# Performance work log

Hardware: AMD Instinct MI355X
Metric: run time of the kernel (lower is better)

Reference implementation:

```python
import jax, jax.numpy as jnp
import numpy as np

GAMMA = 2.0
CONTEXT_WINDOW = 100


def setup_inputs() -> dict:
    key = jax.random.key(0)
    k1, k2 = jax.random.split(key)
    B, S, C = 64, 131072, 3
    inputs = jax.random.normal(k1, (B, S, C), dtype=jnp.float32)
    targets = jax.random.randint(k2, (B, S), 0, C, dtype=jnp.int32)
    alpha = jnp.array([0.25, 1.0, 1.0], dtype=jnp.float32)
    return {"inputs": inputs, "targets": targets, "alpha": alpha}


def _window_mask(targets, window):
    # mask[b, i] = True iff any positive target within +/- window of i;
    # rows with no positives are fully True (matches torch loop semantics).
    B, S = targets.shape
    pos = targets > 0                                   # (B, S) bool
    cs = jnp.cumsum(pos.astype(jnp.int32), axis=1)      # inclusive prefix sums
    c = jnp.concatenate([jnp.zeros((B, 1), jnp.int32), cs], axis=1)  # (B, S+1)
    idx = jnp.arange(S)
    hi = jnp.minimum(idx + window + 1, S)               # exclusive end
    lo = jnp.maximum(idx - window, 0)                   # inclusive start
    count = c[:, hi] - c[:, lo]                         # positives in window
    mask = count > 0
    has_pos = pos.any(axis=1, keepdims=True)
    return jnp.where(has_pos, mask, True)


def reference(inputs, targets, alpha):
    # inputs: (B, S, C) logits; targets: (B, S) class indices
    mask = _window_mask(targets, CONTEXT_WINDOW)                     # (B, S)
    logp = jax.nn.log_softmax(inputs, axis=-1)                       # (B, S, C)
    ce = -jnp.take_along_axis(logp, targets[..., None].astype(jnp.int32), axis=-1)[..., 0]
    p_t = jnp.exp(-ce)
    focal = alpha[targets] * (1.0 - p_t) ** GAMMA * ce               # (B, S)
    m = mask.astype(inputs.dtype)
    # masked mean == mean over selected elements in the torch version
    return jnp.sum(focal * m) / jnp.sum(m)
```

## Files before the change

### kernel.cpp

```cpp
#include <hip/hip_runtime.h>

#define BB 64
#define SS 131072
#define WIN 100
#define TILE 4096
#define NTHREADS 256
#define NWAVES (NTHREADS / 64)
#define TILES_PER_ROW (SS / TILE)
#define NBLOCKS (BB * TILES_PER_ROW)
#define EXT (TILE + 2*WIN)
#define NWORDS ((EXT + 63) / 64)
#define SH_BYTES (NWORDS * 64)
#define K4TOT (SH_BYTES / 4)
#define SROUNDS ((K4TOT + NTHREADS - 1) / NTHREADS)
#define WGROUPS 4
#define GF4 192

typedef float  fx4 __attribute__((ext_vector_type(4)));
typedef int    ix4 __attribute__((ext_vector_type(4)));

__device__ __forceinline__ void process4(
    const fx4 c0, const fx4 c1, const fx4 c2,
    const int j0, const unsigned long long mw, const unsigned int tpack,
    const float a0, const float a1, const float a2,
    float& fsum_m, float& fsum_a, int& cnt_m)
{
    const float xs[12] = {c0.x, c0.y, c0.z, c0.w, c1.x, c1.y, c1.z, c1.w,
                          c2.x, c2.y, c2.z, c2.w};
    #pragma unroll
    for (int j = 0; j < 4; ++j) {
        const float x0 = xs[3*j], x1 = xs[3*j+1], x2 = xs[3*j+2];
        const int tv = (tpack >> (8 * j)) & 0xFF;
        const float mx = fmaxf(x0, fmaxf(x1, x2));
        const float mn = fminf(x0, fminf(x1, x2));
        const float md = fmaxf(fminf(x0, x1), fminf(fmaxf(x0, x1), x2));
        const float emd = __expf(md - mx);
        const float emn = __expf(mn - mx);
        const float sum = 1.0f + emd + emn;
        const float xt  = (tv == 0) ? x0 : ((tv == 1) ? x1 : x2);
        const float et  = (xt == mx) ? 1.0f : ((xt == md) ? emd : emn);
        const float ce  = __logf(sum) + (mx - xt);
        const float pt  = et * __frcp_rn(sum);
        const float w   = (tv == 0) ? a0 : ((tv == 1) ? a1 : a2);
        const float om  = 1.0f - pt;
        const float focal = w * om * om * ce;
        const bool  m   = (mw >> ((j0 & 63) + j)) & 1ULL;

        fsum_a += focal;
        fsum_m += m ? focal : 0.0f;
        cnt_m  += m ? 1 : 0;
    }
}

__global__ __launch_bounds__(NTHREADS, 5) void focal_main(
    const float* __restrict__ inputs, const int* __restrict__ targets,
    const float* __restrict__ alpha, double* __restrict__ slots)
{
    __shared__ __align__(16) unsigned char sh_t[SH_BYTES];
    __shared__ unsigned long long wbits[NWORDS];
    __shared__ unsigned long long mbits[NWORDS];
    __shared__ fx4 lbuf[NWAVES][2][GF4];
    __shared__ double red[NWAVES * 4];

    const int t = threadIdx.x;
    const int w = t >> 6, l = t & 63;
    const int b = blockIdx.x / TILES_PER_ROW;
    const int tile = blockIdx.x % TILES_PER_ROW;
    const int s0 = tile * TILE;
    const int ext_lo = (s0 - WIN > 0) ? (s0 - WIN) : 0;
    const int ext_hi = (s0 + TILE + WIN < SS) ? (s0 + TILE + WIN) : SS;
    const int ext_len = ext_hi - ext_lo;
    const int tr_lo = s0 - ext_lo;

    const float* inrow = inputs + (long)b * SS * 3;
    const fx4* gsrc = (const fx4*)(inrow + (long)(s0 + w * 1024) * 3);
    fx4 q0 = __builtin_nontemporal_load(gsrc + l);
    fx4 q1 = __builtin_nontemporal_load(gsrc + 64 + l);
    fx4 q2 = __builtin_nontemporal_load(gsrc + 128 + l);

    const int* trow = targets + (long)b * SS;
    #pragma unroll
    for (int it = 0; it < SROUNDS; ++it) {
        const int k4 = it * NTHREADS + t;
        if (k4 < K4TOT) {
            unsigned int pk = 0;
            if (4 * k4 < ext_len) {
                const ix4 tv4 =
                    __builtin_nontemporal_load((const ix4*)(trow + ext_lo + 4 * k4));
                pk = (unsigned)(tv4.x & 3) | ((unsigned)(tv4.y & 3) << 8) |
                     ((unsigned)(tv4.z & 3) << 16) | ((unsigned)(tv4.w & 3) << 24);
            }
            ((unsigned int*)sh_t)[k4] = pk;
        }
    }
    __syncthreads();

    int cnt_p = 0;
    if (t < NWORDS) {
        const uint4* qp = (const uint4*)(sh_t + (t << 6));
        unsigned long long wv = 0;
        #pragma unroll
        for (int r = 0; r < 4; ++r) {
            const uint4 u = qp[r];
            unsigned int x, nz;
            x = u.x; nz = (x | (x >> 1)) & 0x01010101u;
            wv |= (unsigned long long)((nz * 0x01020408u) >> 24) << (r*16 + 0);
            x = u.y; nz = (x | (x >> 1)) & 0x01010101u;
            wv |= (unsigned long long)((nz * 0x01020408u) >> 24) << (r*16 + 4);
            x = u.z; nz = (x | (x >> 1)) & 0x01010101u;
            wv |= (unsigned long long)((nz * 0x01020408u) >> 24) << (r*16 + 8);
            x = u.w; nz = (x | (x >> 1)) & 0x01010101u;
            wv |= (unsigned long long)((nz * 0x01020408u) >> 24) << (r*16 + 12);
        }
        wbits[t] = wv;
        int lo_bit = tr_lo - (t << 6);        if (lo_bit < 0) lo_bit = 0;
        int hi_bit = tr_lo + TILE - (t << 6); if (hi_bit > 64) hi_bit = 64;
        if (hi_bit > lo_bit) {
            unsigned long long rm = (hi_bit >= 64) ? ~0ULL : ((1ULL << hi_bit) - 1);
            rm &= (~0ULL << lo_bit);
            cnt_p = __popcll(wv & rm);
        }
    }
    __syncthreads();

    if (t < NWORDS) {
        const unsigned long long a = (t >= 2) ? wbits[t-2] : 0ULL;
        const unsigned long long bw = (t >= 1) ? wbits[t-1] : 0ULL;
        const unsigned long long c = wbits[t];
        const unsigned long long d = (t+1 < NWORDS) ? wbits[t+1] : 0ULL;
        const unsigned long long e = (t+2 < NWORDS) ? wbits[t+2] : 0ULL;
        unsigned long long m = c ? ~0ULL : 0ULL;
        if (d) { const int lo = __builtin_ctzll(d) - 36;
                 m |= (lo <= 0) ? ~0ULL : (~0ULL << lo); }
        if (e) { const int lo = __builtin_ctzll(e) + 28;
                 if (lo <= 63) m |= (~0ULL << lo); }
        if (bw) { const int hi = 63 - __builtin_clzll(bw) + 36;
                  m |= (hi >= 63) ? ~0ULL : (~0ULL >> (63 - hi)); }
        if (a) { const int hi = 63 - __builtin_clzll(a) - 28;
                 if (hi >= 0) m |= (hi >= 63) ? ~0ULL : (~0ULL >> (63 - hi)); }
        mbits[t] = m;
    }
    __syncthreads();

    const float a0 = alpha[0], a1 = alpha[1], a2 = alpha[2];
    float fsum_m = 0.0f, fsum_a = 0.0f;
    int cnt_m = 0;

    #pragma unroll
    for (int g = 0; g < WGROUPS; ++g) {
        fx4* pb = lbuf[w][g & 1];
        pb[l] = q0; pb[64 + l] = q1; pb[128 + l] = q2;
        if (g + 1 < WGROUPS) {
            const fx4* gn = gsrc + (g + 1) * GF4;
            q0 = __builtin_nontemporal_load(gn + l);
            q1 = __builtin_nontemporal_load(gn + 64 + l);
            q2 = __builtin_nontemporal_load(gn + 128 + l);
        }
        const fx4 c0 = pb[3 * l];
        const fx4 c1 = pb[3 * l + 1];
        const fx4 c2 = pb[3 * l + 2];

        const int j0 = tr_lo + w * 1024 + g * 256 + l * 4;
        process4(c0, c1, c2, j0, mbits[j0 >> 6],
                 *(const unsigned int*)(sh_t + j0),
                 a0, a1, a2, fsum_m, fsum_a, cnt_m);
    }

    #pragma unroll
    for (int off = 32; off >= 1; off >>= 1) {
        fsum_m += __shfl_down(fsum_m, off);
        fsum_a += __shfl_down(fsum_a, off);
        cnt_m  += __shfl_down(cnt_m, off);
        cnt_p  += __shfl_down(cnt_p, off);
    }
    if (l == 0) {
        red[w*4]   = (double)fsum_m; red[w*4+1] = (double)cnt_m;
        red[w*4+2] = (double)fsum_a; red[w*4+3] = (double)cnt_p;
    }
    __syncthreads();
    if (t == 0) {
        double sm = 0, sc = 0, sa = 0, sp = 0;
        #pragma unroll
        for (int v = 0; v < NWAVES; ++v) {
            sm += red[v*4]; sc += red[v*4+1]; sa += red[v*4+2]; sp += red[v*4+3];
        }
        double* slot = slots + (long)blockIdx.x * 4;
        slot[0] = sm;
        slot[1] = sc;
        slot[2] = sa;
        slot[3] = sp;
    }
}

__global__ __launch_bounds__(1024) void focal_final(
    const double* __restrict__ slots, float* __restrict__ out)
{
    __shared__ double redA[16 * 2];
    __shared__ double crs[BB];
    __shared__ double crc[BB];
    const int t = threadIdx.x;
    const int wave = t >> 6, lane = t & 63;

    double sm = 0.0, sc = 0.0;
    for (int k = t; k < NBLOCKS; k += 1024) {
        sm += slots[(long)k * 4 + 0];
        sc += slots[(long)k * 4 + 1];
    }
    #pragma unroll
    for (int off = 32; off >= 1; off >>= 1) {
        sm += __shfl_down(sm, off);
        sc += __shfl_down(sc, off);
    }
    if (lane == 0) { redA[wave*2] = sm; redA[wave*2+1] = sc; }

    const int row = t >> 4;
    const int rpart = t & 15;
    const long base = (long)row * TILES_PER_ROW + rpart * 2;
    double rs = slots[base*4 + 2] + slots[(base+1)*4 + 2];
    double rp = slots[base*4 + 3] + slots[(base+1)*4 + 3];
    #pragma unroll
    for (int off = 8; off >= 1; off >>= 1) {
        rs += __shfl_down(rs, off, 16);
        rp += __shfl_down(rp, off, 16);
    }
    if (rpart == 0) { crs[row] = rs; crc[row] = rp; }
    __syncthreads();

    if (t == 0) {
        double a = 0.0, bsum = 0.0;
        #pragma unroll
        for (int v = 0; v < 16; ++v) { a += redA[v*2]; bsum += redA[v*2+1]; }
        double corr_s = 0.0, corr_c = 0.0;
        #pragma unroll
        for (int r = 0; r < BB; ++r) {
            if (crc[r] == 0.0) { corr_s += crs[r]; corr_c += (double)SS; }
        }
        out[0] = (float)((a + corr_s) / (bsum + corr_c));
    }
}

extern "C" void kernel_launch(void* const* d_in, const int* in_sizes, int n_in,
                              void* d_out, int out_size, void* d_ws, size_t ws_size,
                              hipStream_t stream) {
    const float* inputs  = (const float*)d_in[0];
    const int*   targets = (const int*)d_in[1];
    const float* alpha   = (const float*)d_in[2];
    float* out = (float*)d_out;

    double* slots = (double*)d_ws;

    focal_main<<<NBLOCKS, NTHREADS, 0, stream>>>(inputs, targets, alpha, slots);
    focal_final<<<1, 1024, 0, stream>>>(slots, out);
}
```

Measured before the change: 172.0 us.

## Split mask construction into separate kernel writing packed byte metadata

Splits the fused kernel in two. The first kernel builds the window mask from targets and writes one byte per element, holding the target class and the mask bit, to workspace. The second streams the logits together with this metadata, so the main pass no longer carries the shared-memory mask setup and its barriers. The cost is an extra launch and an extra write and read of 8 MB of metadata. It also replaces the reciprocal-based p_t with exp(-ce). A fallback to the fused kernel remains for small workspaces.

```diff
diff --git a/kernel.cpp b/kernel.cpp
--- a/kernel.cpp
+++ b/kernel.cpp
@@ -16,54 +16,22 @@
 #define WGROUPS 4
 #define GF4 192
 
+#define META_OFF 65536
+#define META_BYTES ((size_t)BB * SS)
+
 typedef float  fx4 __attribute__((ext_vector_type(4)));
 typedef int    ix4 __attribute__((ext_vector_type(4)));
 
-__device__ __forceinline__ void process4(
-    const fx4 c0, const fx4 c1, const fx4 c2,
-    const int j0, const unsigned long long mw, const unsigned int tpack,
-    const float a0, const float a1, const float a2,
-    float& fsum_m, float& fsum_a, int& cnt_m)
-{
-    const float xs[12] = {c0.x, c0.y, c0.z, c0.w, c1.x, c1.y, c1.z, c1.w,
-                          c2.x, c2.y, c2.z, c2.w};
-    #pragma unroll
-    for (int j = 0; j < 4; ++j) {
-        const float x0 = xs[3*j], x1 = xs[3*j+1], x2 = xs[3*j+2];
-        const int tv = (tpack >> (8 * j)) & 0xFF;
-        const float mx = fmaxf(x0, fmaxf(x1, x2));
-        const float mn = fminf(x0, fminf(x1, x2));
-        const float md = fmaxf(fminf(x0, x1), fminf(fmaxf(x0, x1), x2));
-        const float emd = __expf(md - mx);
-        const float emn = __expf(mn - mx);
-        const float sum = 1.0f + emd + emn;
-        const float xt  = (tv == 0) ? x0 : ((tv == 1) ? x1 : x2);
-        const float et  = (xt == mx) ? 1.0f : ((xt == md) ? emd : emn);
-        const float ce  = __logf(sum) + (mx - xt);
-        const float pt  = et * __frcp_rn(sum);
-        const float w   = (tv == 0) ? a0 : ((tv == 1) ? a1 : a2);
-        const float om  = 1.0f - pt;
-        const float focal = w * om * om * ce;
-        const bool  m   = (mw >> ((j0 & 63) + j)) & 1ULL;
-
-        fsum_a += focal;
-        fsum_m += m ? focal : 0.0f;
-        cnt_m  += m ? 1 : 0;
-    }
-}
-
-__global__ __launch_bounds__(NTHREADS, 5) void focal_main(
-    const float* __restrict__ inputs, const int* __restrict__ targets,
-    const float* __restrict__ alpha, double* __restrict__ slots)
+__global__ __launch_bounds__(NTHREADS, 8) void mask_build(
+    const int* __restrict__ targets, double* __restrict__ slots,
+    unsigned int* __restrict__ meta)
 {
     __shared__ __align__(16) unsigned char sh_t[SH_BYTES];
     __shared__ unsigned long long wbits[NWORDS];
     __shared__ unsigned long long mbits[NWORDS];
-    __shared__ fx4 lbuf[NWAVES][2][GF4];
-    __shared__ double red[NWAVES * 4];
+    __shared__ int redp[NWAVES];
 
     const int t = threadIdx.x;
-    const int w = t >> 6, l = t & 63;
     const int b = blockIdx.x / TILES_PER_ROW;
     const int tile = blockIdx.x % TILES_PER_ROW;
     const int s0 = tile * TILE;
@@ -71,12 +39,6 @@
     const int ext_hi = (s0 + TILE + WIN < SS) ? (s0 + TILE + WIN) : SS;
     const int ext_len = ext_hi - ext_lo;
     const int tr_lo = s0 - ext_lo;
-
-    const float* inrow = inputs + (long)b * SS * 3;
-    const fx4* gsrc = (const fx4*)(inrow + (long)(s0 + w * 1024) * 3);
-    fx4 q0 = __builtin_nontemporal_load(gsrc + l);
-    fx4 q1 = __builtin_nontemporal_load(gsrc + 64 + l);
-    fx4 q2 = __builtin_nontemporal_load(gsrc + 128 + l);
 
     const int* trow = targets + (long)b * SS;
     #pragma unroll
@@ -142,6 +104,220 @@
     }
     __syncthreads();
 
+    {
+        const unsigned int* shw = (const unsigned int*)sh_t;
+        const int i0 = t << 4;
+        const int j0 = tr_lo + i0;
+        const int wi = j0 >> 6, shv = j0 & 63;
+        unsigned long long mm = mbits[wi] >> shv;
+        if (shv > 48) mm |= mbits[wi + 1] << (64 - shv);
+        const unsigned int m16 = (unsigned int)mm & 0xFFFFu;
+        const int cb = j0 >> 2;
+        uint4 ov;
+        unsigned int s;
+        s = (((m16 >>  0) & 0xFu) * 0x00204081u) & 0x01010101u;
+        ov.x = shw[cb + 0] | (s << 2);
+        s = (((m16 >>  4) & 0xFu) * 0x00204081u) & 0x01010101u;
+        ov.y = shw[cb + 1] | (s << 2);
+        s = (((m16 >>  8) & 0xFu) * 0x00204081u) & 0x01010101u;
+        ov.z = shw[cb + 2] | (s << 2);
+        s = (((m16 >> 12) & 0xFu) * 0x00204081u) & 0x01010101u;
+        ov.w = shw[cb + 3] | (s << 2);
+        *(uint4*)(meta + (long)blockIdx.x * 1024 + (t << 2)) = ov;
+    }
+
+    const int w = t >> 6, l = t & 63;
+    #pragma unroll
+    for (int off = 32; off >= 1; off >>= 1) cnt_p += __shfl_down(cnt_p, off);
+    if (l == 0) redp[w] = cnt_p;
+    __syncthreads();
+    if (t == 0) {
+        slots[(long)blockIdx.x * 4 + 3] =
+            (double)(redp[0] + redp[1] + redp[2] + redp[3]);
+    }
+}
+
+__global__ __launch_bounds__(NTHREADS, 5) void focal_stream(
+    const float* __restrict__ inputs, const unsigned int* __restrict__ meta,
+    const float* __restrict__ alpha, double* __restrict__ slots)
+{
+    __shared__ fx4 lbuf[NWAVES][2][GF4];
+    __shared__ double red[NWAVES * 4];
+
+    const int t = threadIdx.x;
+    const int w = t >> 6, l = t & 63;
+    const int b = blockIdx.x / TILES_PER_ROW;
+    const int tile = blockIdx.x % TILES_PER_ROW;
+    const int s0 = tile * TILE;
+
+    const float* inrow = inputs + (long)b * SS * 3;
+    const fx4* gsrc = (const fx4*)(inrow + (long)(s0 + w * 1024) * 3);
+    const unsigned int* mrow = meta + (long)blockIdx.x * 1024 + w * 256;
+
+    fx4 q0 = __builtin_nontemporal_load(gsrc + l);
+    fx4 q1 = __builtin_nontemporal_load(gsrc + 64 + l);
+    fx4 q2 = __builtin_nontemporal_load(gsrc + 128 + l);
+    unsigned int mg = mrow[l];
+
+    const float a0 = alpha[0], a1 = alpha[1], a2 = alpha[2];
+    float fsum_m = 0.0f, fsum_a = 0.0f;
+    int cnt_m = 0;
+
+    #pragma unroll
+    for (int g = 0; g < WGROUPS; ++g) {
+        fx4* pb = lbuf[w][g & 1];
+        pb[l] = q0; pb[64 + l] = q1; pb[128 + l] = q2;
+        const unsigned int mcur = mg;
+        if (g + 1 < WGROUPS) {
+            const fx4* gn = gsrc + (g + 1) * GF4;
+            q0 = __builtin_nontemporal_load(gn + l);
+            q1 = __builtin_nontemporal_load(gn + 64 + l);
+            q2 = __builtin_nontemporal_load(gn + 128 + l);
+            mg = mrow[(g + 1) * 64 + l];
+        }
+        const fx4 c0 = pb[3 * l];
+        const fx4 c1 = pb[3 * l + 1];
+        const fx4 c2 = pb[3 * l + 2];
+
+        const float xs[12] = {c0.x, c0.y, c0.z, c0.w, c1.x, c1.y, c1.z, c1.w,
+                              c2.x, c2.y, c2.z, c2.w};
+        #pragma unroll
+        for (int j = 0; j < 4; ++j) {
+            const float x0 = xs[3*j], x1 = xs[3*j+1], x2 = xs[3*j+2];
+            const int  tv  = (mcur >> (8 * j)) & 3;
+            const bool msk = (mcur >> (8 * j + 2)) & 1;
+            const float mx = fmaxf(x0, fmaxf(x1, x2));
+            const float mn = fminf(x0, fminf(x1, x2));
+            const float md = fmaxf(fminf(x0, x1), fminf(fmaxf(x0, x1), x2));
+            const float emd = __expf(md - mx);
+            const float emn = __expf(mn - mx);
+            const float sum = 1.0f + emd + emn;
+            const float xt  = (tv == 0) ? x0 : ((tv == 1) ? x1 : x2);
+            const float ce  = __logf(sum) + (mx - xt);
+            const float pt  = __expf(-ce);
+            const float wgt = (tv == 0) ? a0 : ((tv == 1) ? a1 : a2);
+            const float om  = 1.0f - pt;
+            const float focal = wgt * om * om * ce;
+            fsum_a += focal;
+            fsum_m += msk ? focal : 0.0f;
+            cnt_m  += msk ? 1 : 0;
+        }
+    }
+
+    #pragma unroll
+    for (int off = 32; off >= 1; off >>= 1) {
+        fsum_m += __shfl_down(fsum_m, off);
+        fsum_a += __shfl_down(fsum_a, off);
+        cnt_m  += __shfl_down(cnt_m, off);
+    }
+    if (l == 0) {
+        red[w*4]   = (double)fsum_m; red[w*4+1] = (double)cnt_m;
+        red[w*4+2] = (double)fsum_a;
+    }
+    __syncthreads();
+    if (t == 0) {
+        double sm = 0, sc = 0, sa = 0;
+        #pragma unroll
+        for (int v = 0; v < NWAVES; ++v) {
+            sm += red[v*4]; sc += red[v*4+1]; sa += red[v*4+2];
+        }
+        double* slot = slots + (long)blockIdx.x * 4;
+        slot[0] = sm;
+        slot[1] = sc;
+        slot[2] = sa;
+    }
+}
+
+__global__ __launch_bounds__(NTHREADS, 5) void focal_main(
+    const float* __restrict__ inputs, const int* __restrict__ targets,
+    const float* __restrict__ alpha, double* __restrict__ slots)
+{
+    __shared__ __align__(16) unsigned char sh_t[SH_BYTES];
+    __shared__ unsigned long long wbits[NWORDS];
+    __shared__ unsigned long long mbits[NWORDS];
+    __shared__ fx4 lbuf[NWAVES][2][GF4];
+    __shared__ double red[NWAVES * 4];
+
+    const int t = threadIdx.x;
+    const int w = t >> 6, l = t & 63;
+    const int b = blockIdx.x / TILES_PER_ROW;
+    const int tile = blockIdx.x % TILES_PER_ROW;
+    const int s0 = tile * TILE;
+    const int ext_lo = (s0 - WIN > 0) ? (s0 - WIN) : 0;
+    const int ext_hi = (s0 + TILE + WIN < SS) ? (s0 + TILE + WIN) : SS;
+    const int ext_len = ext_hi - ext_lo;
+    const int tr_lo = s0 - ext_lo;
+
+    const float* inrow = inputs + (long)b * SS * 3;
+    const fx4* gsrc = (const fx4*)(inrow + (long)(s0 + w * 1024) * 3);
+    fx4 q0 = __builtin_nontemporal_load(gsrc + l);
+    fx4 q1 = __builtin_nontemporal_load(gsrc + 64 + l);
+    fx4 q2 = __builtin_nontemporal_load(gsrc + 128 + l);
+
+    const int* trow = targets + (long)b * SS;
+    #pragma unroll
+    for (int it = 0; it < SROUNDS; ++it) {
+        const int k4 = it * NTHREADS + t;
+        if (k4 < K4TOT) {
+            unsigned int pk = 0;
+            if (4 * k4 < ext_len) {
+                const ix4 tv4 =
+                    __builtin_nontemporal_load((const ix4*)(trow + ext_lo + 4 * k4));
+                pk = (unsigned)(tv4.x & 3) | ((unsigned)(tv4.y & 3) << 8) |
+                     ((unsigned)(tv4.z & 3) << 16) | ((unsigned)(tv4.w & 3) << 24);
+            }
+            ((unsigned int*)sh_t)[k4] = pk;
+        }
+    }
+    __syncthreads();
+
+    int cnt_p = 0;
+    if (t < NWORDS) {
+        const uint4* qp = (const uint4*)(sh_t + (t << 6));
+        unsigned long long wv = 0;
+        #pragma unroll
+        for (int r = 0; r < 4; ++r) {
+            const uint4 u = qp[r];
+            unsigned int x, nz;
+            x = u.x; nz = (x | (x >> 1)) & 0x01010101u;
+            wv |= (unsigned long long)((nz * 0x01020408u) >> 24) << (r*16 + 0);
+            x = u.y; nz = (x | (x >> 1)) & 0x01010101u;
+            wv |= (unsigned long long)((nz * 0x01020408u) >> 24) << (r*16 + 4);
+            x = u.z; nz = (x | (x >> 1)) & 0x01010101u;
+            wv |= (unsigned long long)((nz * 0x01020408u) >> 24) << (r*16 + 8);
+            x = u.w; nz = (x | (x >> 1)) & 0x01010101u;
+            wv |= (unsigned long long)((nz * 0x01020408u) >> 24) << (r*16 + 12);
+        }
+        wbits[t] = wv;
+        int lo_bit = tr_lo - (t << 6);        if (lo_bit < 0) lo_bit = 0;
+        int hi_bit = tr_lo + TILE - (t << 6); if (hi_bit > 64) hi_bit = 64;
+        if (hi_bit > lo_bit) {
+            unsigned long long rm = (hi_bit >= 64) ? ~0ULL : ((1ULL << hi_bit) - 1);
+            rm &= (~0ULL << lo_bit);
+            cnt_p = __popcll(wv & rm);
+        }
+    }
+    __syncthreads();
+
+    if (t < NWORDS) {
+        const unsigned long long a = (t >= 2) ? wbits[t-2] : 0ULL;
+        const unsigned long long bw = (t >= 1) ? wbits[t-1] : 0ULL;
+        const unsigned long long c = wbits[t];
+        const unsigned long long d = (t+1 < NWORDS) ? wbits[t+1] : 0ULL;
+        const unsigned long long e = (t+2 < NWORDS) ? wbits[t+2] : 0ULL;
+        unsigned long long m = c ? ~0ULL : 0ULL;
+        if (d) { const int lo = __builtin_ctzll(d) - 36;
+                 m |= (lo <= 0) ? ~0ULL : (~0ULL << lo); }
+        if (e) { const int lo = __builtin_ctzll(e) + 28;
+                 if (lo <= 63) m |= (~0ULL << lo); }
+        if (bw) { const int hi = 63 - __builtin_clzll(bw) + 36;
+                  m |= (hi >= 63) ? ~0ULL : (~0ULL >> (63 - hi)); }
+        if (a) { const int hi = 63 - __builtin_clzll(a) - 28;
+                 if (hi >= 0) m |= (hi >= 63) ? ~0ULL : (~0ULL >> (63 - hi)); }
+        mbits[t] = m;
+    }
+    __syncthreads();
+
     const float a0 = alpha[0], a1 = alpha[1], a2 = alpha[2];
     float fsum_m = 0.0f, fsum_a = 0.0f;
     int cnt_m = 0;
@@ -161,9 +337,31 @@
         const fx4 c2 = pb[3 * l + 2];
 
         const int j0 = tr_lo + w * 1024 + g * 256 + l * 4;
-        process4(c0, c1, c2, j0, mbits[j0 >> 6],
-                 *(const unsigned int*)(sh_t + j0),
-                 a0, a1, a2, fsum_m, fsum_a, cnt_m);
+        const unsigned long long mw = mbits[j0 >> 6];
+        const unsigned int tpack = *(const unsigned int*)(sh_t + j0);
+        const float xs[12] = {c0.x, c0.y, c0.z, c0.w, c1.x, c1.y, c1.z, c1.w,
+                              c2.x, c2.y, c2.z, c2.w};
+        #pragma unroll
+        for (int j = 0; j < 4; ++j) {
+            const float x0 = xs[3*j], x1 = xs[3*j+1], x2 = xs[3*j+2];
+            const int tv = (tpack >> (8 * j)) & 0xFF;
+            const float mx = fmaxf(x0, fmaxf(x1, x2));
+            const float mn = fminf(x0, fminf(x1, x2));
+            const float md = fmaxf(fminf(x0, x1), fminf(fmaxf(x0, x1), x2));
+            const float emd = __expf(md - mx);
+            const float emn = __expf(mn - mx);
+            const float sum = 1.0f + emd + emn;
+            const float xt  = (tv == 0) ? x0 : ((tv == 1) ? x1 : x2);
+            const float ce  = __logf(sum) + (mx - xt);
+            const float pt  = __expf(-ce);
+            const float wgt = (tv == 0) ? a0 : ((tv == 1) ? a1 : a2);
+            const float om  = 1.0f - pt;
+            const float focal = wgt * om * om * ce;
+            const bool  msk = (mw >> ((j0 & 63) + j)) & 1ULL;
+            fsum_a += focal;
+            fsum_m += msk ? focal : 0.0f;
+            cnt_m  += msk ? 1 : 0;
+        }
     }
 
     #pragma unroll
@@ -185,10 +383,7 @@
             sm += red[v*4]; sc += red[v*4+1]; sa += red[v*4+2]; sp += red[v*4+3];
         }
         double* slot = slots + (long)blockIdx.x * 4;
-        slot[0] = sm;
-        slot[1] = sc;
-        slot[2] = sa;
-        slot[3] = sp;
+        slot[0] = sm; slot[1] = sc; slot[2] = sa; slot[3] = sp;
     }
 }
 
@@ -249,6 +444,12 @@
 
     double* slots = (double*)d_ws;
 
-    focal_main<<<NBLOCKS, NTHREADS, 0, stream>>>(inputs, targets, alpha, slots);
+    if (ws_size >= META_OFF + META_BYTES) {
+        unsigned int* meta = (unsigned int*)((char*)d_ws + META_OFF);
+        mask_build<<<NBLOCKS, NTHREADS, 0, stream>>>(targets, slots, meta);
+        focal_stream<<<NBLOCKS, NTHREADS, 0, stream>>>(inputs, meta, alpha, slots);
+    } else {
+        focal_main<<<NBLOCKS, NTHREADS, 0, stream>>>(inputs, targets, alpha, slots);
+    }
     focal_final<<<1, 1024, 0, stream>>>(slots, out);
 }
```

Result: no change. 174.7 us (+1.6%).
